# Performance work log

Measured on AMD Instinct MI355X. Metric: run time of the kernel, lower is better.

Reference implementation:

```python
import jax, jax.numpy as jnp
import numpy as np

WINDOW_SIZE = 11
C1 = 0.01 ** 2
C2 = 0.03 ** 2


def _box_filter(x, ws):
    # x: [B,1,H,W]; uniform box filter, zero padding (== torch conv2d pad=ws//2)
    k = jnp.full((1, 1, ws, ws), 1.0 / (ws * ws), dtype=x.dtype)
    pad = ws // 2
    return jax.lax.conv_general_dilated(
        x, k, window_strides=(1, 1), padding=[(pad, pad), (pad, pad)],
        dimension_numbers=('NCHW', 'OIHW', 'NCHW'))


def setup_inputs() -> dict:
    key = jax.random.key(0)
    k1, k2 = jax.random.split(key)
    img1 = jax.random.uniform(k1, (64, 1, 512, 512), dtype=jnp.float32)
    img2 = jax.random.uniform(k2, (64, 1, 512, 512), dtype=jnp.float32)
    return {"img1": img1, "img2": img2}


def reference(img1, img2):
    ws = WINDOW_SIZE
    mu1 = _box_filter(img1, ws)
    mu2 = _box_filter(img2, ws)
    mu1_sq = mu1 * mu1
    mu2_sq = mu2 * mu2
    mu1_mu2 = mu1 * mu2
    sigma1_sq = _box_filter(img1 * img1, ws) - mu1_sq
    sigma2_sq = _box_filter(img2 * img2, ws) - mu2_sq
    sigma12 = _box_filter(img1 * img2, ws) - mu1_mu2
    ssim_map = ((2 * mu1_mu2 + C1) * (2 * sigma12 + C2)) / (
        (mu1_sq + mu2_sq + C1) * (sigma1_sq + sigma2_sq + C2))
    return 1.0 - jnp.mean(ssim_map)
```

## Files before the change

kernel.cpp:

```cpp
#include <hip/hip_runtime.h>


#define IMG_H 512
#define IMG_W 512
#define N_IMG 64
#define STRIP 16
#define NTHREADS 128
#define SSZ 528
#define QSZ 132
#define ROWSZ (SSZ + QSZ)

__global__ __launch_bounds__(NTHREADS) void ssim_kernel(const float* __restrict__ img1,
                                                        const float* __restrict__ img2,
                                                        float* __restrict__ ws) {
    __shared__ __align__(16) float V[2][4][ROWSZ];
    __shared__ float wsum[2];
    const int t = threadIdx.x;
    const int b = blockIdx.y;
    const int r0 = blockIdx.x * STRIP;
    const float* __restrict__ p1 = img1 + (size_t)b * (IMG_H * IMG_W);
    const float* __restrict__ p2 = img2 + (size_t)b * (IMG_H * IMG_W);

    for (int i = t; i < 2 * 4 * ROWSZ; i += NTHREADS) (&V[0][0][0])[i] = 0.0f;

    const int c4 = 4 * t;
    float cs[4][4];
#pragma unroll
    for (int ch = 0; ch < 4; ++ch)
#pragma unroll
        for (int j = 0; j < 4; ++j) cs[ch][j] = 0.0f;

    auto addrow = [&](int r) {
        float4 x = *(const float4*)(p1 + (size_t)r * IMG_W + c4);
        float4 y = *(const float4*)(p2 + (size_t)r * IMG_W + c4);
        float xs[4] = {x.x, x.y, x.z, x.w}, ys[4] = {y.x, y.y, y.z, y.w};
#pragma unroll
        for (int j = 0; j < 4; ++j) {
            float u = xs[j] + ys[j], v = xs[j] - ys[j];
            cs[0][j] += u;                  cs[1][j] += v;
            cs[2][j] = fmaf(u, u, cs[2][j]); cs[3][j] = fmaf(v, v, cs[3][j]);
        }
    };

    float4 pax, pay, psx, psy;
    auto prefetch = [&](int rn) {
        int ra = rn + 5; if (ra > IMG_H - 1) ra = IMG_H - 1;
        int rs = rn - 6; if (rs < 0) rs = 0;
        pax = *(const float4*)(p1 + (size_t)ra * IMG_W + c4);
        pay = *(const float4*)(p2 + (size_t)ra * IMG_W + c4);
        psx = *(const float4*)(p1 + (size_t)rs * IMG_W + c4);
        psy = *(const float4*)(p2 + (size_t)rs * IMG_W + c4);
    };
    auto consume = [&](int rn) {
        if (rn + 5 < IMG_H) {
            float xs[4] = {pax.x, pax.y, pax.z, pax.w};
            float ys[4] = {pay.x, pay.y, pay.z, pay.w};
#pragma unroll
            for (int j = 0; j < 4; ++j) {
                float u = xs[j] + ys[j], v = xs[j] - ys[j];
                cs[0][j] += u;                  cs[1][j] += v;
                cs[2][j] = fmaf(u, u, cs[2][j]); cs[3][j] = fmaf(v, v, cs[3][j]);
            }
        }
        if (rn - 6 >= 0) {
            float xs[4] = {psx.x, psx.y, psx.z, psx.w};
            float ys[4] = {psy.x, psy.y, psy.z, psy.w};
#pragma unroll
            for (int j = 0; j < 4; ++j) {
                float u = xs[j] + ys[j], v = xs[j] - ys[j];
                cs[0][j] -= u;                  cs[1][j] -= v;
                cs[2][j] = fmaf(-u, u, cs[2][j]); cs[3][j] = fmaf(-v, v, cs[3][j]);
            }
        }
    };
    auto writeSQ = [&](int p) {
#pragma unroll
        for (int ch = 0; ch < 4; ++ch) {
            *(float4*)&V[p][ch][8 + c4] =
                make_float4(cs[ch][0], cs[ch][1], cs[ch][2], cs[ch][3]);
            V[p][ch][SSZ + 2 + t] = (cs[ch][0] + cs[ch][1]) + (cs[ch][2] + cs[ch][3]);
        }
    };

    int offS[4][3], offQ[4][2];
#pragma unroll
    for (int k = 0; k < 4; ++k) {
        const int c = t + 128 * k;
        const int rho = c & 3;
        int e0, e1, e2;
        if (rho == 0)      { e0 = -5; e1 =  4; e2 =  5; }
        else if (rho == 1) { e0 =  3; e1 =  4; e2 =  5; }
        else if (rho == 2) { e0 = -5; e1 = -4; e2 = -3; }
        else               { e0 = -5; e1 = -4; e2 =  5; }
        offS[k][0] = c + 8 + e0; offS[k][1] = c + 8 + e1; offS[k][2] = c + 8 + e2;
        const int mlo = (c >> 2) + ((rho < 2) ? -1 : 0);
        offQ[k][0] = SSZ + 2 + mlo; offQ[k][1] = SSZ + 3 + mlo;
    }

    {
        int rlo = r0 - 5; if (rlo < 0) rlo = 0;
        const int rhi = r0 + 5;
        for (int r = rlo; r <= rhi; ++r) addrow(r);
    }
    __syncthreads();
    writeSQ(0);
    prefetch(r0 + 1);
    __syncthreads();

    constexpr float inv  = 1.0f / 121.0f;
    constexpr float inv2 = 0.5f / 121.0f;
    constexpr float C1c = 0.01f * 0.01f;
    constexpr float C2c = 0.03f * 0.03f;
    float acc = 0.0f;

    auto hphase = [&](int p) {
        const float* __restrict__ Vf = &V[p][0][0];
#pragma unroll
        for (int k = 0; k < 4; ++k) {
            float W[4];
#pragma unroll
            for (int ch = 0; ch < 4; ++ch) {
                const int base = ch * ROWSZ;
                W[ch] = ((Vf[base + offS[k][0]] + Vf[base + offS[k][1]]) +
                         (Vf[base + offS[k][2]] + Vf[base + offQ[k][0]])) +
                        Vf[base + offQ[k][1]];
            }
            float mu_u = W[0] * inv, mu_v = W[1] * inv;
            float uu = mu_u * mu_u, vv = mu_v * mu_v;
            float P = 0.5f * (uu + vv);
            float M = 0.5f * (uu - vv);
            float A = fmaf(W[2] + W[3], inv2, -P);
            float B = fmaf(W[2] - W[3], inv2, -M);
            float num = (M + C1c) * (B + C2c);
            float den = (P + C1c) * (A + C2c);
            acc += __fdividef(num, den);
        }
    };

    for (int i = 0; i < STRIP - 1; ++i) {
        consume(r0 + i + 1);
        int rn = r0 + i + 2;
        if (rn > r0 + STRIP - 1) rn = r0 + STRIP - 1;
        prefetch(rn);
        writeSQ((i + 1) & 1);
        hphase(i & 1);
        __syncthreads();
    }
    hphase((STRIP - 1) & 1);

#pragma unroll
    for (int off = 32; off > 0; off >>= 1) acc += __shfl_down(acc, off);
    if ((t & 63) == 0) wsum[t >> 6] = acc;
    __syncthreads();
    if (t == 0) atomicAdd(ws, wsum[0] + wsum[1]);
}

__global__ void ssim_finalize(const float* __restrict__ ws, float* __restrict__ out) {
    constexpr float inv_n = 1.0f / (float)((size_t)N_IMG * IMG_H * IMG_W);
    out[0] = 1.0f - ws[0] * inv_n;
}

extern "C" void kernel_launch(void* const* d_in, const int* in_sizes, int n_in,
                              void* d_out, int out_size, void* d_ws, size_t ws_size,
                              hipStream_t stream) {
    const float* img1 = (const float*)d_in[0];
    const float* img2 = (const float*)d_in[1];
    float* out = (float*)d_out;
    float* ws = (float*)d_ws;

    hipMemsetAsync(ws, 0, sizeof(float), stream);

    dim3 grid(IMG_H / STRIP, N_IMG);
    ssim_kernel<<<grid, NTHREADS, 0, stream>>>(img1, img2, ws);
    ssim_finalize<<<1, 1, 0, stream>>>(ws, out);
}
```

Baseline: 192.8 us.

## Split each row strip into two column halves with halo columns, doubling strip height

Each block now covers a 32-row by 256-column tile instead of a 16-row full-width strip, so every thread handles two columns instead of four. Threads 0-7 also load halo column pairs on either side of the tile. This shrinks per-thread registers and shared memory and amortises the 10-row vertical warm-up over twice as many output rows. The cost is extra halo loads and cross-lane shuffles to build the quad sums, plus fewer loads per thread to hide latency.

```diff
diff --git a/kernel.cpp b/kernel.cpp
--- a/kernel.cpp
+++ b/kernel.cpp
@@ -4,10 +4,11 @@
 #define IMG_H 512
 #define IMG_W 512
 #define N_IMG 64
-#define STRIP 16
+#define STRIP 32
+#define BCOLS 256
 #define NTHREADS 128
-#define SSZ 528
-#define QSZ 132
+#define SSZ 272
+#define QSZ 68
 #define ROWSZ (SSZ + QSZ)
 
 __global__ __launch_bounds__(NTHREADS) void ssim_kernel(const float* __restrict__ img1,
@@ -17,91 +18,118 @@
     __shared__ float wsum[2];
     const int t = threadIdx.x;
     const int b = blockIdx.y;
-    const int r0 = blockIdx.x * STRIP;
+    const int sx = blockIdx.x >> 1;
+    const int half = blockIdx.x & 1;
+    const int r0 = sx * STRIP;
+    const int cbase = half * BCOLS;
     const float* __restrict__ p1 = img1 + (size_t)b * (IMG_H * IMG_W);
     const float* __restrict__ p2 = img2 + (size_t)b * (IMG_H * IMG_W);
 
     for (int i = t; i < 2 * 4 * ROWSZ; i += NTHREADS) (&V[0][0][0])[i] = 0.0f;
 
-    const int c4 = 4 * t;
-    float cs[4][4];
+    const int cm = cbase + 2 * t;
+    const int hloc = (t < 4) ? (-8 + 2 * t) : (256 + 2 * (t - 4));
+    const int hcol = cbase + hloc;
+    const bool hval = (t < 8) && (hcol >= 0) && (hcol <= IMG_W - 2);
+
+    float cs[4][2], csH[4][2];
 #pragma unroll
     for (int ch = 0; ch < 4; ++ch)
 #pragma unroll
-        for (int j = 0; j < 4; ++j) cs[ch][j] = 0.0f;
-
-    auto addrow = [&](int r) {
-        float4 x = *(const float4*)(p1 + (size_t)r * IMG_W + c4);
-        float4 y = *(const float4*)(p2 + (size_t)r * IMG_W + c4);
-        float xs[4] = {x.x, x.y, x.z, x.w}, ys[4] = {y.x, y.y, y.z, y.w};
-#pragma unroll
-        for (int j = 0; j < 4; ++j) {
-            float u = xs[j] + ys[j], v = xs[j] - ys[j];
-            cs[0][j] += u;                  cs[1][j] += v;
-            cs[2][j] = fmaf(u, u, cs[2][j]); cs[3][j] = fmaf(v, v, cs[3][j]);
-        }
-    };
-
-    float4 pax, pay, psx, psy;
+        for (int j = 0; j < 2; ++j) { cs[ch][j] = 0.0f; csH[ch][j] = 0.0f; }
+
+    auto addPair = [&](float (&a)[4][2], float2 x, float2 y) {
+#pragma unroll
+        for (int j = 0; j < 2; ++j) {
+            float xv = j ? x.y : x.x, yv = j ? y.y : y.x;
+            float u = xv + yv, v = xv - yv;
+            a[0][j] += u;                   a[1][j] += v;
+            a[2][j] = fmaf(u, u, a[2][j]);  a[3][j] = fmaf(v, v, a[3][j]);
+        }
+    };
+    auto subPair = [&](float (&a)[4][2], float2 x, float2 y) {
+#pragma unroll
+        for (int j = 0; j < 2; ++j) {
+            float xv = j ? x.y : x.x, yv = j ? y.y : y.x;
+            float u = xv + yv, v = xv - yv;
+            a[0][j] -= u;                   a[1][j] -= v;
+            a[2][j] = fmaf(-u, u, a[2][j]); a[3][j] = fmaf(-v, v, a[3][j]);
+        }
+    };
+
+    {
+        int rlo = r0 - 5; if (rlo < 0) rlo = 0;
+        const int rhi = r0 + 5;
+        for (int r = rlo; r <= rhi; ++r) {
+            float2 x = *(const float2*)(p1 + (size_t)r * IMG_W + cm);
+            float2 y = *(const float2*)(p2 + (size_t)r * IMG_W + cm);
+            addPair(cs, x, y);
+            if (hval) {
+                float2 hx = *(const float2*)(p1 + (size_t)r * IMG_W + hcol);
+                float2 hy = *(const float2*)(p2 + (size_t)r * IMG_W + hcol);
+                addPair(csH, hx, hy);
+            }
+        }
+    }
+
+    float2 pax, pay, psx, psy, hax, hay, hsx, hsy;
     auto prefetch = [&](int rn) {
         int ra = rn + 5; if (ra > IMG_H - 1) ra = IMG_H - 1;
         int rs = rn - 6; if (rs < 0) rs = 0;
-        pax = *(const float4*)(p1 + (size_t)ra * IMG_W + c4);
-        pay = *(const float4*)(p2 + (size_t)ra * IMG_W + c4);
-        psx = *(const float4*)(p1 + (size_t)rs * IMG_W + c4);
-        psy = *(const float4*)(p2 + (size_t)rs * IMG_W + c4);
+        pax = *(const float2*)(p1 + (size_t)ra * IMG_W + cm);
+        pay = *(const float2*)(p2 + (size_t)ra * IMG_W + cm);
+        psx = *(const float2*)(p1 + (size_t)rs * IMG_W + cm);
+        psy = *(const float2*)(p2 + (size_t)rs * IMG_W + cm);
+        if (hval) {
+            hax = *(const float2*)(p1 + (size_t)ra * IMG_W + hcol);
+            hay = *(const float2*)(p2 + (size_t)ra * IMG_W + hcol);
+            hsx = *(const float2*)(p1 + (size_t)rs * IMG_W + hcol);
+            hsy = *(const float2*)(p2 + (size_t)rs * IMG_W + hcol);
+        }
     };
     auto consume = [&](int rn) {
         if (rn + 5 < IMG_H) {
-            float xs[4] = {pax.x, pax.y, pax.z, pax.w};
-            float ys[4] = {pay.x, pay.y, pay.z, pay.w};
-#pragma unroll
-            for (int j = 0; j < 4; ++j) {
-                float u = xs[j] + ys[j], v = xs[j] - ys[j];
-                cs[0][j] += u;                  cs[1][j] += v;
-                cs[2][j] = fmaf(u, u, cs[2][j]); cs[3][j] = fmaf(v, v, cs[3][j]);
+            addPair(cs, pax, pay);
+            if (hval) addPair(csH, hax, hay);
+        }
+        if (rn - 6 >= 0) {
+            subPair(cs, psx, psy);
+            if (hval) subPair(csH, hsx, hsy);
+        }
+    };
+
+    auto writeSQ = [&](int p) {
+#pragma unroll
+        for (int ch = 0; ch < 4; ++ch) {
+            *(float2*)&V[p][ch][8 + 2 * t] = make_float2(cs[ch][0], cs[ch][1]);
+            float ps = cs[ch][0] + cs[ch][1];
+            float nb = __shfl_down(ps, 1);
+            if ((t & 1) == 0) V[p][ch][SSZ + 2 + (t >> 1)] = ps + nb;
+            float psH = csH[ch][0] + csH[ch][1];
+            float nbH = __shfl_down(psH, 1);
+            if (t < 8) {
+                *(float2*)&V[p][ch][8 + hloc] = make_float2(csH[ch][0], csH[ch][1]);
+                if ((t & 1) == 0) {
+                    const int qi = (t < 4) ? (t >> 1) : (64 + (t >> 1));
+                    V[p][ch][SSZ + qi] = psH + nbH;
+                }
             }
         }
-        if (rn - 6 >= 0) {
-            float xs[4] = {psx.x, psx.y, psx.z, psx.w};
-            float ys[4] = {psy.x, psy.y, psy.z, psy.w};
-#pragma unroll
-            for (int j = 0; j < 4; ++j) {
-                float u = xs[j] + ys[j], v = xs[j] - ys[j];
-                cs[0][j] -= u;                  cs[1][j] -= v;
-                cs[2][j] = fmaf(-u, u, cs[2][j]); cs[3][j] = fmaf(-v, v, cs[3][j]);
-            }
-        }
-    };
-    auto writeSQ = [&](int p) {
-#pragma unroll
-        for (int ch = 0; ch < 4; ++ch) {
-            *(float4*)&V[p][ch][8 + c4] =
-                make_float4(cs[ch][0], cs[ch][1], cs[ch][2], cs[ch][3]);
-            V[p][ch][SSZ + 2 + t] = (cs[ch][0] + cs[ch][1]) + (cs[ch][2] + cs[ch][3]);
-        }
-    };
-
-    int offS[4][3], offQ[4][2];
-#pragma unroll
-    for (int k = 0; k < 4; ++k) {
-        const int c = t + 128 * k;
-        const int rho = c & 3;
+    };
+
+    int sOff[3], q0;
+    {
+        const int rho = t & 3;
         int e0, e1, e2;
         if (rho == 0)      { e0 = -5; e1 =  4; e2 =  5; }
         else if (rho == 1) { e0 =  3; e1 =  4; e2 =  5; }
         else if (rho == 2) { e0 = -5; e1 = -4; e2 = -3; }
         else               { e0 = -5; e1 = -4; e2 =  5; }
-        offS[k][0] = c + 8 + e0; offS[k][1] = c + 8 + e1; offS[k][2] = c + 8 + e2;
-        const int mlo = (c >> 2) + ((rho < 2) ? -1 : 0);
-        offQ[k][0] = SSZ + 2 + mlo; offQ[k][1] = SSZ + 3 + mlo;
+        sOff[0] = t + 8 + e0; sOff[1] = t + 8 + e1; sOff[2] = t + 8 + e2;
+        const int mlo = (t >> 2) + ((rho < 2) ? -1 : 0);
+        q0 = SSZ + 2 + mlo;
     }
 
-    {
-        int rlo = r0 - 5; if (rlo < 0) rlo = 0;
-        const int rhi = r0 + 5;
-        for (int r = rlo; r <= rhi; ++r) addrow(r);
-    }
     __syncthreads();
     writeSQ(0);
     prefetch(r0 + 1);
@@ -114,16 +142,16 @@
     float acc = 0.0f;
 
     auto hphase = [&](int p) {
-        const float* __restrict__ Vf = &V[p][0][0];
-#pragma unroll
-        for (int k = 0; k < 4; ++k) {
+#pragma unroll
+        for (int k = 0; k < 2; ++k) {
+            const int ds = 128 * k, dq = 32 * k;
             float W[4];
 #pragma unroll
             for (int ch = 0; ch < 4; ++ch) {
-                const int base = ch * ROWSZ;
-                W[ch] = ((Vf[base + offS[k][0]] + Vf[base + offS[k][1]]) +
-                         (Vf[base + offS[k][2]] + Vf[base + offQ[k][0]])) +
-                        Vf[base + offQ[k][1]];
+                const float* __restrict__ Vf = &V[p][ch][0];
+                W[ch] = ((Vf[sOff[0] + ds] + Vf[sOff[1] + ds]) +
+                         (Vf[sOff[2] + ds] + Vf[q0 + dq])) +
+                        Vf[q0 + 1 + dq];
             }
             float mu_u = W[0] * inv, mu_v = W[1] * inv;
             float uu = mu_u * mu_u, vv = mu_v * mu_v;
@@ -170,7 +198,7 @@
 
     hipMemsetAsync(ws, 0, sizeof(float), stream);
 
-    dim3 grid(IMG_H / STRIP, N_IMG);
+    dim3 grid((IMG_H / STRIP) * 2, N_IMG);
     ssim_kernel<<<grid, NTHREADS, 0, stream>>>(img1, img2, ws);
     ssim_finalize<<<1, 1, 0, stream>>>(ws, out);
 }
```

Result: faster. 183.7 us (-4.7%).
